# Optimization experiments

Measured on AMD Instinct MI355X. Metric: run time of the kernel, lower is better.

The kernel has to match this reference:

```python
import jax, jax.numpy as jnp
import numpy as np

B, L, C = 128, 1000, 12      # batch, seq_len, input_channels
H = 128                       # lstm_hidden
DM, DS, DC = 128, 16, 4       # d_model, d_state, d_conv
DI = 2 * DM                   # d_inner = expand * d_model
DR = 8                        # dt_rank = ceil(d_model/16)
FC, NC = 128, 5               # fc_hidden_size, num_classes


def setup_inputs() -> dict:
    key = jax.random.key(0)
    ks = jax.random.split(key, 24)
    def rn(k, shape, fan):
        return jax.random.normal(k, shape, jnp.float32) / np.sqrt(fan)
    inp = {}
    inp["x"] = jax.random.normal(ks[0], (B, L, C), jnp.float32)
    # LSTM (single layer, batch_first) — PyTorch gate order i,f,g,o
    inp["W_ih"] = rn(ks[1], (4 * H, C), H)
    inp["W_hh"] = rn(ks[2], (4 * H, H), H)
    inp["b_ih"] = rn(ks[3], (4 * H,), H)
    inp["b_hh"] = rn(ks[4], (4 * H,), H)
    # input_proj: Linear(H, DM)
    inp["Wp"] = rn(ks[5], (DM, H), H)
    inp["bp"] = rn(ks[6], (DM,), H)
    # Mamba params
    inp["in_proj_w"] = rn(ks[7], (2 * DI, DM), DM)
    inp["conv_w"] = rn(ks[8], (DI, 1, DC), DC)        # depthwise conv kernel
    inp["conv_b"] = rn(ks[9], (DI,), DC)
    inp["x_proj_w"] = rn(ks[10], (DR + 2 * DS, DI), DI)
    inp["dt_proj_w"] = rn(ks[11], (DI, DR), DR)
    inp["dt_proj_b"] = rn(ks[12], (DI,), DR)
    inp["A_log"] = jnp.broadcast_to(jnp.log(jnp.arange(1, DS + 1, dtype=jnp.float32)), (DI, DS)).copy()
    inp["D"] = jnp.ones((DI,), jnp.float32)
    inp["out_proj_w"] = rn(ks[13], (DM, DI), DI)
    # classifier head
    inp["fc1_w"] = rn(ks[14], (FC, DM), DM)
    inp["fc1_b"] = rn(ks[15], (FC,), DM)
    inp["fc2_w"] = rn(ks[16], (NC, FC), FC)
    inp["fc2_b"] = rn(ks[17], (NC,), FC)
    return inp


def _lstm(x, W_ih, W_hh, b_ih, b_hh):
    b = b_ih + b_hh
    xg = jnp.einsum('blc,gc->blg', x, W_ih) + b  # precompute input gates (B,L,4H)
    def step(carry, xt):
        h, c = carry
        g = xt + h @ W_hh.T
        i, f, gg, o = jnp.split(g, 4, axis=-1)
        c = jax.nn.sigmoid(f) * c + jax.nn.sigmoid(i) * jnp.tanh(gg)
        h = jax.nn.sigmoid(o) * jnp.tanh(c)
        return (h, c), h
    h0 = jnp.zeros((x.shape[0], H), x.dtype)
    (_, _), hs = jax.lax.scan(step, (h0, h0), jnp.swapaxes(xg, 0, 1))
    return jnp.swapaxes(hs, 0, 1)  # (B,L,H)


def _mamba(u, in_proj_w, conv_w, conv_b, x_proj_w, dt_proj_w, dt_proj_b, A_log, D, out_proj_w):
    xz = jnp.einsum('bld,ed->ble', u, in_proj_w)           # (B,L,2*DI)
    xi, z = jnp.split(xz, 2, axis=-1)
    # causal depthwise conv1d over time
    xc = jnp.swapaxes(xi, 1, 2)                             # (B,DI,L)
    xc = jax.lax.conv_general_dilated(xc, conv_w, (1,), [(DC - 1, 0)],
                                      feature_group_count=DI,
                                      dimension_numbers=('NCH', 'OIH', 'NCH'))
    xc = xc + conv_b[None, :, None]
    xs = jax.nn.silu(jnp.swapaxes(xc, 1, 2))                # (B,L,DI)
    x_dbl = jnp.einsum('bld,ed->ble', xs, x_proj_w)         # (B,L,DR+2*DS)
    dt, Bm, Cm = jnp.split(x_dbl, [DR, DR + DS], axis=-1)
    delta = jax.nn.softplus(jnp.einsum('blr,dr->bld', dt, dt_proj_w) + dt_proj_b)  # (B,L,DI)
    A = -jnp.exp(A_log)                                     # (DI,DS)
    def step(h, inp):
        d_t, B_t, C_t, x_t = inp                            # (B,DI),(B,DS),(B,DS),(B,DI)
        dA = jnp.exp(d_t[:, :, None] * A)                   # (B,DI,DS)
        h = dA * h + (d_t * x_t)[:, :, None] * B_t[:, None, :]
        y = jnp.einsum('bds,bs->bd', h, C_t)
        return h, y
    h0 = jnp.zeros((u.shape[0], DI, DS), u.dtype)
    seq = (jnp.swapaxes(delta, 0, 1), jnp.swapaxes(Bm, 0, 1),
           jnp.swapaxes(Cm, 0, 1), jnp.swapaxes(xs, 0, 1))
    _, ys = jax.lax.scan(step, h0, seq)                     # (L,B,DI)
    y = jnp.swapaxes(ys, 0, 1) + xs * D
    y = y * jax.nn.silu(z)
    return jnp.einsum('bld,ed->ble', y, out_proj_w)         # (B,L,DM)


def reference(x, W_ih, W_hh, b_ih, b_hh, Wp, bp, in_proj_w, conv_w, conv_b,
              x_proj_w, dt_proj_w, dt_proj_b, A_log, D, out_proj_w,
              fc1_w, fc1_b, fc2_w, fc2_b):
    h = _lstm(x, W_ih, W_hh, b_ih, b_hh)
    m_in = jnp.einsum('blh,dh->bld', h, Wp) + bp
    m_out = _mamba(m_in, in_proj_w, conv_w, conv_b, x_proj_w,
                   dt_proj_w, dt_proj_b, A_log, D, out_proj_w)
    pooled = m_out.mean(axis=1)                             # (B,DM)
    hfc = jax.nn.relu(pooled @ fc1_w.T + fc1_b)             # dropout: eval mode (identity)
    return hfc @ fc2_w.T + fc2_b                            # (B,NC)
```

## Files before the change

kernel.cpp:

```cpp
#include <hip/hip_runtime.h>
#include <cstdint>
#include <cstddef>

constexpr int LSEQ = 1000;
constexpr int NB   = 128;
constexpr int CINP = 12;
constexpr int HID  = 128;
constexpr int NGATE = 4 * HID;
constexpr int DMOD = 128;
constexpr int DINN = 256;
constexpr int NCL  = 5;

typedef unsigned short ushort_t;
typedef _Float16 half2_t __attribute__((ext_vector_type(2)));

__device__ __forceinline__ float bf2f(ushort_t u) {
  uint32_t b = ((uint32_t)u) << 16;
  float f; __builtin_memcpy(&f, &b, 4); return f;
}
__device__ __forceinline__ ushort_t f2bf(float f) {
  uint32_t b; __builtin_memcpy(&b, &f, 4);
  uint32_t r = (b + 0x7fffu + ((b >> 16) & 1u)) >> 16;
  return (ushort_t)r;
}
__device__ __forceinline__ half2_t u2h2(uint32_t v) {
  half2_t h; __builtin_memcpy(&h, &v, 4); return h;
}
__device__ __forceinline__ uint32_t h22u(half2_t h) {
  uint32_t v; __builtin_memcpy(&v, &h, 4); return v;
}
__device__ __forceinline__ uint32_t bfpair_to_h2(uint32_t v) {
  half2_t h;
  h.x = (_Float16)bf2f((ushort_t)(v & 0xffff));
  h.y = (_Float16)bf2f((ushort_t)(v >> 16));
  return h22u(h);
}

#if __has_builtin(__builtin_amdgcn_fdot2)
__device__ __forceinline__ float FDOT2(half2_t a, half2_t b, float c) {
  return __builtin_amdgcn_fdot2(a, b, c, false);
}
#else
__device__ __forceinline__ float FDOT2(half2_t a, half2_t b, float c) {
  return c + (float)a.x * (float)b.x + (float)a.y * (float)b.y;
}
#endif

__device__ __forceinline__ void bar_lgkm() {
  asm volatile("s_waitcnt lgkmcnt(0)\n\ts_barrier" ::: "memory");
}

__global__ __launch_bounds__(256) void k0_weff(
    const float* __restrict__ ipw, const float* __restrict__ Wp,
    const float* __restrict__ bp, uint32_t* __restrict__ Weffh,
    float* __restrict__ beff) {
  int idx = blockIdx.x * 256 + threadIdx.x;
  if (idx < NGATE * 64) {
    int e = idx >> 6, j = idx & 63;
    float a0 = 0.f, a1 = 0.f;
    for (int d = 0; d < DMOD; ++d) {
      float w = ipw[e * DMOD + d];
      a0 += w * Wp[d * HID + 2 * j];
      a1 += w * Wp[d * HID + 2 * j + 1];
    }
    half2_t h; h.x = (_Float16)a0; h.y = (_Float16)a1;
    Weffh[idx] = h22u(h);
  }
  if (idx < NGATE) {
    float acc = 0.f;
    for (int d = 0; d < DMOD; ++d) acc += ipw[idx * DMOD + d] * bp[d];
    beff[idx] = acc;
  }
}

__global__ __launch_bounds__(256, 1) void k1_lstm(
    const float* __restrict__ x, const float* __restrict__ W_ih,
    const float* __restrict__ W_hh, const float* __restrict__ b_ih,
    const float* __restrict__ b_hh, ushort_t* __restrict__ hout) {
  __shared__ __align__(16) float x_sh[LSEQ * CINP];
  __shared__ __align__(16) ushort_t h_sh[HID];
  __shared__ float tg_sh[HID];
  __shared__ float so_sh[HID];
  const int t = threadIdx.x;
  const int u = t & 127;
  const int half = t >> 7;
  const int rA = u + half * 256;
  const int rB = rA + 128;
  const int b = blockIdx.x;

  const float4* xg4 = reinterpret_cast<const float4*>(x + (size_t)b * LSEQ * CINP);
  float4* xs4 = reinterpret_cast<float4*>(x_sh);
  for (int i = t; i < LSEQ * CINP / 4; i += 256) xs4[i] = xg4[i];

  half2_t wa2[64], wb2[64];
  {
    const float4* wa4 = reinterpret_cast<const float4*>(W_hh) + rA * (HID / 4);
    const float4* wb4 = reinterpret_cast<const float4*>(W_hh) + rB * (HID / 4);
#pragma unroll
    for (int k = 0; k < HID / 4; ++k) {
      float4 v = wa4[k];
      half2_t a; a.x = (_Float16)v.x; a.y = (_Float16)v.y;
      half2_t c; c.x = (_Float16)v.z; c.y = (_Float16)v.w;
      wa2[2 * k] = a; wa2[2 * k + 1] = c;
      float4 w = wb4[k];
      half2_t d; d.x = (_Float16)w.x; d.y = (_Float16)w.y;
      half2_t e; e.x = (_Float16)w.z; e.y = (_Float16)w.w;
      wb2[2 * k] = d; wb2[2 * k + 1] = e;
    }
  }
  float wia[CINP], wib[CINP];
#pragma unroll
  for (int c = 0; c < CINP; ++c) {
    wia[c] = W_ih[rA * CINP + c];
    wib[c] = W_ih[rB * CINP + c];
  }
  const float biasA = b_ih[rA] + b_hh[rA];
  const float biasB = b_ih[rB] + b_hh[rB];

  float cstate = 0.f;
  if (t < HID) h_sh[t] = 0;
  __syncthreads();

  for (int l = 0; l < LSEQ; ++l) {
    const float* xr = &x_sh[l * CINP];
    float pa0 = biasA, pa1 = 0.f, pa2 = 0.f, pa3 = 0.f;
    float pb0 = biasB, pb1 = 0.f, pb2 = 0.f, pb3 = 0.f;
#pragma unroll
    for (int c = 0; c < CINP; c += 4) {
      float x0 = xr[c], x1 = xr[c + 1], x2 = xr[c + 2], x3 = xr[c + 3];
      pa0 += x0 * wia[c];     pa1 += x1 * wia[c + 1];
      pa2 += x2 * wia[c + 2]; pa3 += x3 * wia[c + 3];
      pb0 += x0 * wib[c];     pb1 += x1 * wib[c + 1];
      pb2 += x2 * wib[c + 2]; pb3 += x3 * wib[c + 3];
    }
    const uint4* h4 = reinterpret_cast<const uint4*>(h_sh);
#pragma unroll
    for (int kk = 0; kk < 16; ++kk) {
      uint4 hv = h4[kk];
      half2_t h0 = u2h2(hv.x), h1 = u2h2(hv.y), h2 = u2h2(hv.z), h3 = u2h2(hv.w);
      pa0 = FDOT2(h0, wa2[4 * kk],     pa0);
      pa1 = FDOT2(h1, wa2[4 * kk + 1], pa1);
      pa2 = FDOT2(h2, wa2[4 * kk + 2], pa2);
      pa3 = FDOT2(h3, wa2[4 * kk + 3], pa3);
      pb0 = FDOT2(h0, wb2[4 * kk],     pb0);
      pb1 = FDOT2(h1, wb2[4 * kk + 1], pb1);
      pb2 = FDOT2(h2, wb2[4 * kk + 2], pb2);
      pb3 = FDOT2(h3, wb2[4 * kk + 3], pb3);
    }
    float gA = (pa0 + pa1) + (pa2 + pa3);
    float gB = (pb0 + pb1) + (pb2 + pb3);

    float si = 0.f, sf = 0.f;
    if (half) {
      float tg = 1.f - 2.f / (__expf(2.f * gA) + 1.f);
      float so = 1.f / (1.f + __expf(-gB));
      tg_sh[u] = tg;
      so_sh[u] = so;
    } else {
      si = 1.f / (1.f + __expf(-gA));
      sf = 1.f / (1.f + __expf(-gB));
    }
    bar_lgkm();
    if (!half) {
      cstate = sf * cstate + si * tg_sh[u];
      float th = 1.f - 2.f / (__expf(2.f * cstate) + 1.f);
      float hv = so_sh[u] * th;
      _Float16 hh = (_Float16)hv;
      ushort_t hb; __builtin_memcpy(&hb, &hh, 2);
      h_sh[u] = hb;
      hout[((size_t)b * LSEQ + l) * HID + u] = f2bf(hv);
    }
    bar_lgkm();
  }
}

__global__ __launch_bounds__(256) void k2_xz(
    const ushort_t* __restrict__ hbuf, const uint32_t* __restrict__ Weffh,
    const float* __restrict__ beff, ushort_t* __restrict__ xi,
    ushort_t* __restrict__ sz) {
  constexpr int S = 66;
  __shared__ __align__(16) uint32_t As[64 * S];
  __shared__ __align__(16) uint32_t Bs[64 * S];
  const int tid = threadIdx.x;
  const size_t m0 = (size_t)blockIdx.x * 64;
  const int n0 = blockIdx.y * 64;

  const uint4* h4g = reinterpret_cast<const uint4*>(hbuf);
  for (int i = tid; i < 64 * 16; i += 256) {
    int row = i >> 4, c = i & 15;
    uint4 v = h4g[(m0 + row) * 16 + c];
    uint32_t* p = &As[row * S + c * 4];
    p[0] = bfpair_to_h2(v.x); p[1] = bfpair_to_h2(v.y);
    p[2] = bfpair_to_h2(v.z); p[3] = bfpair_to_h2(v.w);
  }
  const uint4* w4g = reinterpret_cast<const uint4*>(Weffh);
  for (int i = tid; i < 64 * 16; i += 256) {
    int row = i >> 4, c = i & 15;
    uint4 v = w4g[(size_t)(n0 + row) * 16 + c];
    uint32_t* p = &Bs[row * S + c * 4];
    p[0] = v.x; p[1] = v.y; p[2] = v.z; p[3] = v.w;
  }
  __syncthreads();

  const int tx = tid & 15, ty = tid >> 4;
  float acc[4][4] = {};
  const uint32_t* ap = &As[(ty * 4) * S];
  const uint32_t* bp = &Bs[(tx * 4) * S];
#pragma unroll 4
  for (int kk = 0; kk < 32; ++kk) {
    uint2 a0 = *reinterpret_cast<const uint2*>(&ap[kk * 2]);
    uint2 a1 = *reinterpret_cast<const uint2*>(&ap[S + kk * 2]);
    uint2 a2 = *reinterpret_cast<const uint2*>(&ap[2 * S + kk * 2]);
    uint2 a3 = *reinterpret_cast<const uint2*>(&ap[3 * S + kk * 2]);
    uint2 b0 = *reinterpret_cast<const uint2*>(&bp[kk * 2]);
    uint2 b1 = *reinterpret_cast<const uint2*>(&bp[S + kk * 2]);
    uint2 b2 = *reinterpret_cast<const uint2*>(&bp[2 * S + kk * 2]);
    uint2 b3 = *reinterpret_cast<const uint2*>(&bp[3 * S + kk * 2]);
    acc[0][0] = FDOT2(u2h2(a0.x), u2h2(b0.x), acc[0][0]);
    acc[0][1] = FDOT2(u2h2(a0.x), u2h2(b1.x), acc[0][1]);
    acc[0][2] = FDOT2(u2h2(a0.x), u2h2(b2.x), acc[0][2]);
    acc[0][3] = FDOT2(u2h2(a0.x), u2h2(b3.x), acc[0][3]);
    acc[1][0] = FDOT2(u2h2(a1.x), u2h2(b0.x), acc[1][0]);
    acc[1][1] = FDOT2(u2h2(a1.x), u2h2(b1.x), acc[1][1]);
    acc[1][2] = FDOT2(u2h2(a1.x), u2h2(b2.x), acc[1][2]);
    acc[1][3] = FDOT2(u2h2(a1.x), u2h2(b3.x), acc[1][3]);
    acc[2][0] = FDOT2(u2h2(a2.x), u2h2(b0.x), acc[2][0]);
    acc[2][1] = FDOT2(u2h2(a2.x), u2h2(b1.x), acc[2][1]);
    acc[2][2] = FDOT2(u2h2(a2.x), u2h2(b2.x), acc[2][2]);
    acc[2][3] = FDOT2(u2h2(a2.x), u2h2(b3.x), acc[2][3]);
    acc[3][0] = FDOT2(u2h2(a3.x), u2h2(b0.x), acc[3][0]);
    acc[3][1] = FDOT2(u2h2(a3.x), u2h2(b1.x), acc[3][1]);
    acc[3][2] = FDOT2(u2h2(a3.x), u2h2(b2.x), acc[3][2]);
    acc[3][3] = FDOT2(u2h2(a3.x), u2h2(b3.x), acc[3][3]);
    acc[0][0] = FDOT2(u2h2(a0.y), u2h2(b0.y), acc[0][0]);
    acc[0][1] = FDOT2(u2h2(a0.y), u2h2(b1.y), acc[0][1]);
    acc[0][2] = FDOT2(u2h2(a0.y), u2h2(b2.y), acc[0][2]);
    acc[0][3] = FDOT2(u2h2(a0.y), u2h2(b3.y), acc[0][3]);
    acc[1][0] = FDOT2(u2h2(a1.y), u2h2(b0.y), acc[1][0]);
    acc[1][1] = FDOT2(u2h2(a1.y), u2h2(b1.y), acc[1][1]);
    acc[1][2] = FDOT2(u2h2(a1.y), u2h2(b2.y), acc[1][2]);
    acc[1][3] = FDOT2(u2h2(a1.y), u2h2(b3.y), acc[1][3]);
    acc[2][0] = FDOT2(u2h2(a2.y), u2h2(b0.y), acc[2][0]);
    acc[2][1] = FDOT2(u2h2(a2.y), u2h2(b1.y), acc[2][1]);
    acc[2][2] = FDOT2(u2h2(a2.y), u2h2(b2.y), acc[2][2]);
    acc[2][3] = FDOT2(u2h2(a2.y), u2h2(b3.y), acc[2][3]);
    acc[3][0] = FDOT2(u2h2(a3.y), u2h2(b0.y), acc[3][0]);
    acc[3][1] = FDOT2(u2h2(a3.y), u2h2(b1.y), acc[3][1]);
    acc[3][2] = FDOT2(u2h2(a3.y), u2h2(b2.y), acc[3][2]);
    acc[3][3] = FDOT2(u2h2(a3.y), u2h2(b3.y), acc[3][3]);
  }

  const int col = n0 + tx * 4;
  float4 be = *reinterpret_cast<const float4*>(&beff[col]);
#pragma unroll
  for (int i = 0; i < 4; ++i) {
    size_t row = m0 + ty * 4 + i;
    float v0 = acc[i][0] + be.x, v1 = acc[i][1] + be.y;
    float v2 = acc[i][2] + be.z, v3 = acc[i][3] + be.w;
    ushort4 o;
    if (n0 < 256) {
      o.x = f2bf(v0); o.y = f2bf(v1); o.z = f2bf(v2); o.w = f2bf(v3);
      *reinterpret_cast<ushort4*>(&xi[row * 256 + col]) = o;
    } else {
      o.x = f2bf(v0 / (1.f + __expf(-v0)));
      o.y = f2bf(v1 / (1.f + __expf(-v1)));
      o.z = f2bf(v2 / (1.f + __expf(-v2)));
      o.w = f2bf(v3 / (1.f + __expf(-v3)));
      *reinterpret_cast<ushort4*>(&sz[row * 256 + (col - 256)]) = o;
    }
  }
}

__global__ __launch_bounds__(256) void k3_conv(
    const ushort_t* __restrict__ xi, const float* __restrict__ cw,
    const float* __restrict__ cb, ushort_t* __restrict__ xs) {
  const int d = threadIdx.x;
  const size_t bl0 = (size_t)blockIdx.x * 4;
  const int l0 = (int)(bl0 % LSEQ);
  float w0 = cw[d * 4], w1 = cw[d * 4 + 1], w2 = cw[d * 4 + 2], w3 = cw[d * 4 + 3];
  const float cbv = cb[d];
  const ushort_t* p = &xi[bl0 * 256 + d];
  float xm3 = (l0 >= 3) ? bf2f(p[-768]) : 0.f;
  float xm2 = (l0 >= 2) ? bf2f(p[-512]) : 0.f;
  float xm1 = (l0 >= 1) ? bf2f(p[-256]) : 0.f;
  float x0 = bf2f(p[0]);
  float x1 = bf2f(p[256]);
  float x2 = bf2f(p[512]);
  float x3 = bf2f(p[768]);
  float o0 = cbv + w0 * xm3 + w1 * xm2 + w2 * xm1 + w3 * x0;
  float o1 = cbv + w0 * xm2 + w1 * xm1 + w2 * x0 + w3 * x1;
  float o2 = cbv + w0 * xm1 + w1 * x0 + w2 * x1 + w3 * x2;
  float o3 = cbv + w0 * x0 + w1 * x1 + w2 * x2 + w3 * x3;
  ushort_t* q = &xs[bl0 * 256 + d];
  q[0]   = f2bf(o0 / (1.f + __expf(-o0)));
  q[256] = f2bf(o1 / (1.f + __expf(-o1)));
  q[512] = f2bf(o2 / (1.f + __expf(-o2)));
  q[768] = f2bf(o3 / (1.f + __expf(-o3)));
}

__global__ __launch_bounds__(256) void k4_xdbl(
    const ushort_t* __restrict__ xs, const float* __restrict__ xpw,
    float* __restrict__ dtg, float* __restrict__ bc) {
  constexpr int XSTR = 134;
  __shared__ __align__(16) uint32_t xsh[64 * XSTR];
  __shared__ __align__(16) uint32_t wsh[40 * 128];
  const int tid = threadIdx.x;
  const size_t r0 = (size_t)blockIdx.x * 64;

  for (int i = tid; i < 64 * 128; i += 256) {
    int row = i >> 7, kk = i & 127;
    uint32_t v = *reinterpret_cast<const uint32_t*>(&xs[(r0 + row) * 256 + kk * 2]);
    xsh[row * XSTR + kk] = bfpair_to_h2(v);
  }
  for (int i = tid; i < 40 * 128; i += 256) {
    int c = i >> 7, kk = i & 127;
    half2_t h;
    h.x = (_Float16)xpw[c * 256 + kk * 2];
    h.y = (_Float16)xpw[c * 256 + kk * 2 + 1];
    wsh[i] = h22u(h);
  }
  __syncthreads();

  const int row = tid & 63;
  const int cg = tid >> 6;
  float acc[10] = {};
  for (int kk2 = 0; kk2 < 64; ++kk2) {
    uint2 xv = *reinterpret_cast<const uint2*>(&xsh[row * XSTR + kk2 * 2]);
    half2_t x0 = u2h2(xv.x), x1 = u2h2(xv.y);
#pragma unroll
    for (int i = 0; i < 10; ++i) {
      uint2 wv = *reinterpret_cast<const uint2*>(&wsh[(cg + 4 * i) * 128 + kk2 * 2]);
      acc[i] = FDOT2(x0, u2h2(wv.x), acc[i]);
      acc[i] = FDOT2(x1, u2h2(wv.y), acc[i]);
    }
  }
#pragma unroll
  for (int i = 0; i < 10; ++i) {
    int c = cg + 4 * i;
    if (c < 8) dtg[(r0 + row) * 8 + c] = acc[i];
    else bc[(r0 + row) * 32 + (c - 8)] = acc[i];
  }
}

__global__ __launch_bounds__(256) void k5_scan(
    const float* __restrict__ dtg, const ushort_t* __restrict__ xs,
    const ushort_t* __restrict__ sz, const float* __restrict__ bc,
    const float* __restrict__ A_log, const float* __restrict__ Dv,
    const float* __restrict__ dtw, const float* __restrict__ dtb,
    float* __restrict__ ysum) {
  const int b  = blockIdx.x >> 3;
  const int d  = ((blockIdx.x & 7) << 5) + (threadIdx.x >> 3);
  const int sg = threadIdx.x & 7;

  const float Aa0 = -__expf(A_log[d * 16 + sg * 2]);
  const float Aa1 = -__expf(A_log[d * 16 + sg * 2 + 1]);
  float w8[8];
#pragma unroll
  for (int r = 0; r < 8; ++r) w8[r] = dtw[d * 8 + r];
  const float db = dtb[d];
  const float DD = Dv[d];

  float h0 = 0.f, h1 = 0.f;
  float acc = 0.f, accD = 0.f;
  const size_t base = (size_t)b * LSEQ;

  float4 dta_c = *reinterpret_cast<const float4*>(&dtg[base * 8]);
  float4 dtb_c = *reinterpret_cast<const float4*>(&dtg[base * 8 + 4]);
  float  xv_c  = bf2f(xs[base * 256 + d]);
  float  zv_c  = bf2f(sz[base * 256 + d]);
  float2 bv_c  = *reinterpret_cast<const float2*>(&bc[base * 32 + sg * 2]);
  float2 cv_c  = *reinterpret_cast<const float2*>(&bc[base * 32 + 16 + sg * 2]);

  for (int l = 0; l < LSEQ; ++l) {
    const size_t nrow = base + ((l + 1 < LSEQ) ? (l + 1) : l);
    float4 dta_n = *reinterpret_cast<const float4*>(&dtg[nrow * 8]);
    float4 dtb_n = *reinterpret_cast<const float4*>(&dtg[nrow * 8 + 4]);
    float  xv_n  = bf2f(xs[nrow * 256 + d]);
    float  zv_n  = bf2f(sz[nrow * 256 + d]);
    float2 bv_n  = *reinterpret_cast<const float2*>(&bc[nrow * 32 + sg * 2]);
    float2 cv_n  = *reinterpret_cast<const float2*>(&bc[nrow * 32 + 16 + sg * 2]);

    float a = db + dta_c.x * w8[0] + dta_c.y * w8[1] + dta_c.z * w8[2] + dta_c.w * w8[3]
                 + dtb_c.x * w8[4] + dtb_c.y * w8[5] + dtb_c.z * w8[6] + dtb_c.w * w8[7];
    float dl = (a > 20.f) ? a : __logf(1.f + __expf(a));
    float dx = dl * xv_c;
    h0 = __expf(dl * Aa0) * h0 + dx * bv_c.x;
    h1 = __expf(dl * Aa1) * h1 + dx * bv_c.y;
    acc += (h0 * cv_c.x + h1 * cv_c.y) * zv_c;
    accD += xv_c * zv_c;

    dta_c = dta_n; dtb_c = dtb_n;
    xv_c = xv_n; zv_c = zv_n; bv_c = bv_n; cv_c = cv_n;
  }
  if (sg == 0) acc += DD * accD;
  acc += __shfl_xor(acc, 1);
  acc += __shfl_xor(acc, 2);
  acc += __shfl_xor(acc, 4);
  if (sg == 0) ysum[b * 256 + d] = acc;
}

__global__ __launch_bounds__(128) void k6_head(
    const float* __restrict__ ysum, const float* __restrict__ opw,
    const float* __restrict__ fc1w, const float* __restrict__ fc1b,
    const float* __restrict__ fc2w, const float* __restrict__ fc2b,
    float* __restrict__ out) {
  __shared__ float ys[256], pool[128], fcs[128];
  const int b = blockIdx.x, t = threadIdx.x;
  for (int i = t; i < 256; i += 128) ys[i] = ysum[b * 256 + i];
  __syncthreads();
  float a = 0.f;
  for (int e = 0; e < 256; ++e) a += opw[t * 256 + e] * ys[e];
  pool[t] = a * (1.0f / (float)LSEQ);
  __syncthreads();
  float a1 = fc1b[t];
  for (int d2 = 0; d2 < 128; ++d2) a1 += fc1w[t * 128 + d2] * pool[d2];
  fcs[t] = fmaxf(a1, 0.f);
  __syncthreads();
  if (t < NCL) {
    float o = fc2b[t];
    for (int f = 0; f < 128; ++f) o += fc2w[t * 128 + f] * fcs[f];
    out[b * NCL + t] = o;
  }
}

extern "C" void kernel_launch(void* const* d_in, const int* in_sizes, int n_in,
                              void* d_out, int out_size, void* d_ws, size_t ws_size,
                              hipStream_t stream) {
  const float* x     = (const float*)d_in[0];
  const float* W_ih  = (const float*)d_in[1];
  const float* W_hh  = (const float*)d_in[2];
  const float* b_ih  = (const float*)d_in[3];
  const float* b_hh  = (const float*)d_in[4];
  const float* Wp    = (const float*)d_in[5];
  const float* bp    = (const float*)d_in[6];
  const float* ipw   = (const float*)d_in[7];
  const float* cw    = (const float*)d_in[8];
  const float* cb    = (const float*)d_in[9];
  const float* xpw   = (const float*)d_in[10];
  const float* dtw   = (const float*)d_in[11];
  const float* dtb   = (const float*)d_in[12];
  const float* A_log = (const float*)d_in[13];
  const float* Dv    = (const float*)d_in[14];
  const float* opw   = (const float*)d_in[15];
  const float* fc1w  = (const float*)d_in[16];
  const float* fc1b  = (const float*)d_in[17];
  const float* fc2w  = (const float*)d_in[18];
  const float* fc2b  = (const float*)d_in[19];
  float* out = (float*)d_out;

  const size_t A_WEFF = 131072;
  const size_t A_BEFF = 4096, A_YSUM = 131072;
  const size_t A_HBUF = (size_t)NB * LSEQ * HID * 2;
  const size_t A_XS   = (size_t)NB * LSEQ * DINN * 2;
  const size_t A_SZ   = A_XS;
  const size_t A_DT   = (size_t)NB * LSEQ * 8 * 4;
  const size_t A_BC   = (size_t)NB * LSEQ * 32 * 4;
  const size_t FIXED_WIDE = A_WEFF + A_BEFF + A_YSUM + A_HBUF + A_XS + A_SZ + A_DT + A_BC;

  int nb_w = 0;
  for (int c = 128; c >= 8; c >>= 1) {
    if (FIXED_WIDE + (size_t)c * LSEQ * DINN * 2 <= ws_size) { nb_w = c; break; }
  }

  if (nb_w > 0) {
    char* p = (char*)d_ws;
    uint32_t* Weffh = (uint32_t*)p; p += A_WEFF;
    float*    beff = (float*)p;    p += A_BEFF;
    float*    ysum = (float*)p;    p += A_YSUM;
    ushort_t* hbuf = (ushort_t*)p; p += A_HBUF;
    ushort_t* xsb  = (ushort_t*)p; p += A_XS;
    ushort_t* szb  = (ushort_t*)p; p += A_SZ;
    float*    dtg  = (float*)p;    p += A_DT;
    float*    bcb  = (float*)p;    p += A_BC;
    ushort_t* xib  = (ushort_t*)p;

    hipLaunchKernelGGL(k0_weff, dim3(128), dim3(256), 0, stream, ipw, Wp, bp, Weffh, beff);
    hipLaunchKernelGGL(k1_lstm, dim3(NB), dim3(256), 0, stream, x, W_ih, W_hh, b_ih, b_hh, hbuf);

    for (int b0 = 0; b0 < NB; b0 += nb_w) {
      const int rows = nb_w * LSEQ;
      const size_t ro = (size_t)b0 * LSEQ;
      hipLaunchKernelGGL(k2_xz, dim3(rows / 64, 8), dim3(256), 0, stream,
                         hbuf + ro * HID, Weffh, beff, xib, szb + ro * DINN);
      hipLaunchKernelGGL(k3_conv, dim3(rows / 4), dim3(256), 0, stream,
                         xib, cw, cb, xsb + ro * DINN);
      hipLaunchKernelGGL(k4_xdbl, dim3(rows / 64), dim3(256), 0, stream,
                         xsb + ro * DINN, xpw, dtg + ro * 8, bcb + ro * 32);
    }
    hipLaunchKernelGGL(k5_scan, dim3(NB * 8), dim3(256), 0, stream,
                       dtg, xsb, szb, bcb, A_log, Dv, dtw, dtb, ysum);
    hipLaunchKernelGGL(k6_head, dim3(NB), dim3(128), 0, stream,
                       ysum, opw, fc1w, fc1b, fc2w, fc2b, out);
    return;
  }

  const size_t FIXED = A_WEFF + A_BEFF + A_YSUM + A_HBUF;
  const size_t PERB = (size_t)LSEQ * DINN * 2 * 3 + (size_t)LSEQ * 8 * 4 + (size_t)LSEQ * 32 * 4;
  int nb = 8;
  for (int c = 128; c >= 8; c >>= 1) {
    if (FIXED + (size_t)c * PERB <= ws_size) { nb = c; break; }
  }
  char* p = (char*)d_ws;
  uint32_t* Weffh = (uint32_t*)p; p += A_WEFF;
  float*    beff = (float*)p;    p += A_BEFF;
  float*    ysum = (float*)p;    p += A_YSUM;
  ushort_t* hbuf = (ushort_t*)p; p += A_HBUF;
  ushort_t* xib  = (ushort_t*)p; p += (size_t)nb * LSEQ * DINN * 2;
  ushort_t* szb  = (ushort_t*)p; p += (size_t)nb * LSEQ * DINN * 2;
  ushort_t* xsb  = (ushort_t*)p; p += (size_t)nb * LSEQ * DINN * 2;
  float*    dtg  = (float*)p;    p += (size_t)nb * LSEQ * 8 * 4;
  float*    bcb  = (float*)p;

  hipLaunchKernelGGL(k0_weff, dim3(128), dim3(256), 0, stream, ipw, Wp, bp, Weffh, beff);
  hipLaunchKernelGGL(k1_lstm, dim3(NB), dim3(256), 0, stream, x, W_ih, W_hh, b_ih, b_hh, hbuf);
  for (int b0 = 0; b0 < NB; b0 += nb) {
    const int rows = nb * LSEQ;
    hipLaunchKernelGGL(k2_xz, dim3(rows / 64, 8), dim3(256), 0, stream,
                       hbuf + (size_t)b0 * LSEQ * HID, Weffh, beff, xib, szb);
    hipLaunchKernelGGL(k3_conv, dim3(rows / 4), dim3(256), 0, stream, xib, cw, cb, xsb);
    hipLaunchKernelGGL(k4_xdbl, dim3(rows / 64), dim3(256), 0, stream, xsb, xpw, dtg, bcb);
    hipLaunchKernelGGL(k5_scan, dim3(nb * 8), dim3(256), 0, stream,
                       dtg, xsb, szb, bcb, A_log, Dv, dtw, dtb, ysum + (size_t)b0 * DINN);
  }
  hipLaunchKernelGGL(k6_head, dim3(NB), dim3(128), 0, stream,
                     ysum, opw, fc1w, fc1b, fc2w, fc2b, out);
}
```

Before: 1.507 ms.

## Fuse depthwise causal conv and SiLU into the x/z projection GEMM epilogue

```diff
diff --git a/kernel.cpp b/kernel.cpp
--- a/kernel.cpp
+++ b/kernel.cpp
@@ -174,13 +174,15 @@
   }
 }
 
-__global__ __launch_bounds__(256) void k2_xz(
+__global__ __launch_bounds__(256) void k2f(
     const ushort_t* __restrict__ hbuf, const uint32_t* __restrict__ Weffh,
-    const float* __restrict__ beff, ushort_t* __restrict__ xi,
+    const float* __restrict__ beff, const float* __restrict__ cw,
+    const float* __restrict__ cb, ushort_t* __restrict__ xs,
     ushort_t* __restrict__ sz) {
   constexpr int S = 66;
-  __shared__ __align__(16) uint32_t As[64 * S];
-  __shared__ __align__(16) uint32_t Bs[64 * S];
+  __shared__ __align__(16) uint32_t smem[2 * 64 * S];
+  uint32_t* As = smem;
+  uint32_t* Bs = smem + 64 * S;
   const int tid = threadIdx.x;
   const size_t m0 = (size_t)blockIdx.x * 64;
   const int n0 = blockIdx.y * 64;
@@ -204,98 +206,132 @@
 
   const int tx = tid & 15, ty = tid >> 4;
   float acc[4][4] = {};
-  const uint32_t* ap = &As[(ty * 4) * S];
-  const uint32_t* bp = &Bs[(tx * 4) * S];
+  {
+    const uint32_t* ap = &As[(ty * 4) * S];
+    const uint32_t* bp = &Bs[(tx * 4) * S];
 #pragma unroll 4
-  for (int kk = 0; kk < 32; ++kk) {
-    uint2 a0 = *reinterpret_cast<const uint2*>(&ap[kk * 2]);
-    uint2 a1 = *reinterpret_cast<const uint2*>(&ap[S + kk * 2]);
-    uint2 a2 = *reinterpret_cast<const uint2*>(&ap[2 * S + kk * 2]);
-    uint2 a3 = *reinterpret_cast<const uint2*>(&ap[3 * S + kk * 2]);
-    uint2 b0 = *reinterpret_cast<const uint2*>(&bp[kk * 2]);
-    uint2 b1 = *reinterpret_cast<const uint2*>(&bp[S + kk * 2]);
-    uint2 b2 = *reinterpret_cast<const uint2*>(&bp[2 * S + kk * 2]);
-    uint2 b3 = *reinterpret_cast<const uint2*>(&bp[3 * S + kk * 2]);
-    acc[0][0] = FDOT2(u2h2(a0.x), u2h2(b0.x), acc[0][0]);
-    acc[0][1] = FDOT2(u2h2(a0.x), u2h2(b1.x), acc[0][1]);
-    acc[0][2] = FDOT2(u2h2(a0.x), u2h2(b2.x), acc[0][2]);
-    acc[0][3] = FDOT2(u2h2(a0.x), u2h2(b3.x), acc[0][3]);
-    acc[1][0] = FDOT2(u2h2(a1.x), u2h2(b0.x), acc[1][0]);
-    acc[1][1] = FDOT2(u2h2(a1.x), u2h2(b1.x), acc[1][1]);
-    acc[1][2] = FDOT2(u2h2(a1.x), u2h2(b2.x), acc[1][2]);
-    acc[1][3] = FDOT2(u2h2(a1.x), u2h2(b3.x), acc[1][3]);
-    acc[2][0] = FDOT2(u2h2(a2.x), u2h2(b0.x), acc[2][0]);
-    acc[2][1] = FDOT2(u2h2(a2.x), u2h2(b1.x), acc[2][1]);
-    acc[2][2] = FDOT2(u2h2(a2.x), u2h2(b2.x), acc[2][2]);
-    acc[2][3] = FDOT2(u2h2(a2.x), u2h2(b3.x), acc[2][3]);
-    acc[3][0] = FDOT2(u2h2(a3.x), u2h2(b0.x), acc[3][0]);
-    acc[3][1] = FDOT2(u2h2(a3.x), u2h2(b1.x), acc[3][1]);
-    acc[3][2] = FDOT2(u2h2(a3.x), u2h2(b2.x), acc[3][2]);
-    acc[3][3] = FDOT2(u2h2(a3.x), u2h2(b3.x), acc[3][3]);
-    acc[0][0] = FDOT2(u2h2(a0.y), u2h2(b0.y), acc[0][0]);
-    acc[0][1] = FDOT2(u2h2(a0.y), u2h2(b1.y), acc[0][1]);
-    acc[0][2] = FDOT2(u2h2(a0.y), u2h2(b2.y), acc[0][2]);
-    acc[0][3] = FDOT2(u2h2(a0.y), u2h2(b3.y), acc[0][3]);
-    acc[1][0] = FDOT2(u2h2(a1.y), u2h2(b0.y), acc[1][0]);
-    acc[1][1] = FDOT2(u2h2(a1.y), u2h2(b1.y), acc[1][1]);
-    acc[1][2] = FDOT2(u2h2(a1.y), u2h2(b2.y), acc[1][2]);
-    acc[1][3] = FDOT2(u2h2(a1.y), u2h2(b3.y), acc[1][3]);
-    acc[2][0] = FDOT2(u2h2(a2.y), u2h2(b0.y), acc[2][0]);
-    acc[2][1] = FDOT2(u2h2(a2.y), u2h2(b1.y), acc[2][1]);
-    acc[2][2] = FDOT2(u2h2(a2.y), u2h2(b2.y), acc[2][2]);
-    acc[2][3] = FDOT2(u2h2(a2.y), u2h2(b3.y), acc[2][3]);
-    acc[3][0] = FDOT2(u2h2(a3.y), u2h2(b0.y), acc[3][0]);
-    acc[3][1] = FDOT2(u2h2(a3.y), u2h2(b1.y), acc[3][1]);
-    acc[3][2] = FDOT2(u2h2(a3.y), u2h2(b2.y), acc[3][2]);
-    acc[3][3] = FDOT2(u2h2(a3.y), u2h2(b3.y), acc[3][3]);
+    for (int kk = 0; kk < 32; ++kk) {
+      uint2 a0 = *reinterpret_cast<const uint2*>(&ap[kk * 2]);
+      uint2 a1 = *reinterpret_cast<const uint2*>(&ap[S + kk * 2]);
+      uint2 a2 = *reinterpret_cast<const uint2*>(&ap[2 * S + kk * 2]);
+      uint2 a3 = *reinterpret_cast<const uint2*>(&ap[3 * S + kk * 2]);
+      uint2 b0 = *reinterpret_cast<const uint2*>(&bp[kk * 2]);
+      uint2 b1 = *reinterpret_cast<const uint2*>(&bp[S + kk * 2]);
+      uint2 b2 = *reinterpret_cast<const uint2*>(&bp[2 * S + kk * 2]);
+      uint2 b3 = *reinterpret_cast<const uint2*>(&bp[3 * S + kk * 2]);
+      acc[0][0] = FDOT2(u2h2(a0.x), u2h2(b0.x), acc[0][0]);
+      acc[0][1] = FDOT2(u2h2(a0.x), u2h2(b1.x), acc[0][1]);
+      acc[0][2] = FDOT2(u2h2(a0.x), u2h2(b2.x), acc[0][2]);
+      acc[0][3] = FDOT2(u2h2(a0.x), u2h2(b3.x), acc[0][3]);
+      acc[1][0] = FDOT2(u2h2(a1.x), u2h2(b0.x), acc[1][0]);
+      acc[1][1] = FDOT2(u2h2(a1.x), u2h2(b1.x), acc[1][1]);
+      acc[1][2] = FDOT2(u2h2(a1.x), u2h2(b2.x), acc[1][2]);
+      acc[1][3] = FDOT2(u2h2(a1.x), u2h2(b3.x), acc[1][3]);
+      acc[2][0] = FDOT2(u2h2(a2.x), u2h2(b0.x), acc[2][0]);
+      acc[2][1] = FDOT2(u2h2(a2.x), u2h2(b1.x), acc[2][1]);
+      acc[2][2] = FDOT2(u2h2(a2.x), u2h2(b2.x), acc[2][2]);
+      acc[2][3] = FDOT2(u2h2(a2.x), u2h2(b3.x), acc[2][3]);
+      acc[3][0] = FDOT2(u2h2(a3.x), u2h2(b0.x), acc[3][0]);
+      acc[3][1] = FDOT2(u2h2(a3.x), u2h2(b1.x), acc[3][1]);
+      acc[3][2] = FDOT2(u2h2(a3.x), u2h2(b2.x), acc[3][2]);
+      acc[3][3] = FDOT2(u2h2(a3.x), u2h2(b3.x), acc[3][3]);
+      acc[0][0] = FDOT2(u2h2(a0.y), u2h2(b0.y), acc[0][0]);
+      acc[0][1] = FDOT2(u2h2(a0.y), u2h2(b1.y), acc[0][1]);
+      acc[0][2] = FDOT2(u2h2(a0.y), u2h2(b2.y), acc[0][2]);
+      acc[0][3] = FDOT2(u2h2(a0.y), u2h2(b3.y), acc[0][3]);
+      acc[1][0] = FDOT2(u2h2(a1.y), u2h2(b0.y), acc[1][0]);
+      acc[1][1] = FDOT2(u2h2(a1.y), u2h2(b1.y), acc[1][1]);
+      acc[1][2] = FDOT2(u2h2(a1.y), u2h2(b2.y), acc[1][2]);
+      acc[1][3] = FDOT2(u2h2(a1.y), u2h2(b3.y), acc[1][3]);
+      acc[2][0] = FDOT2(u2h2(a2.y), u2h2(b0.y), acc[2][0]);
+      acc[2][1] = FDOT2(u2h2(a2.y), u2h2(b1.y), acc[2][1]);
+      acc[2][2] = FDOT2(u2h2(a2.y), u2h2(b2.y), acc[2][2]);
+      acc[2][3] = FDOT2(u2h2(a2.y), u2h2(b3.y), acc[2][3]);
+      acc[3][0] = FDOT2(u2h2(a3.y), u2h2(b0.y), acc[3][0]);
+      acc[3][1] = FDOT2(u2h2(a3.y), u2h2(b1.y), acc[3][1]);
+      acc[3][2] = FDOT2(u2h2(a3.y), u2h2(b2.y), acc[3][2]);
+      acc[3][3] = FDOT2(u2h2(a3.y), u2h2(b3.y), acc[3][3]);
+    }
   }
 
   const int col = n0 + tx * 4;
   float4 be = *reinterpret_cast<const float4*>(&beff[col]);
-#pragma unroll
-  for (int i = 0; i < 4; ++i) {
-    size_t row = m0 + ty * 4 + i;
-    float v0 = acc[i][0] + be.x, v1 = acc[i][1] + be.y;
-    float v2 = acc[i][2] + be.z, v3 = acc[i][3] + be.w;
-    ushort4 o;
-    if (n0 < 256) {
-      o.x = f2bf(v0); o.y = f2bf(v1); o.z = f2bf(v2); o.w = f2bf(v3);
-      *reinterpret_cast<ushort4*>(&xi[row * 256 + col]) = o;
-    } else {
+
+  if (n0 >= 256) {
+#pragma unroll
+    for (int i = 0; i < 4; ++i) {
+      size_t row = m0 + ty * 4 + i;
+      float v0 = acc[i][0] + be.x, v1 = acc[i][1] + be.y;
+      float v2 = acc[i][2] + be.z, v3 = acc[i][3] + be.w;
+      ushort4 o;
       o.x = f2bf(v0 / (1.f + __expf(-v0)));
       o.y = f2bf(v1 / (1.f + __expf(-v1)));
       o.z = f2bf(v2 / (1.f + __expf(-v2)));
       o.w = f2bf(v3 / (1.f + __expf(-v3)));
       *reinterpret_cast<ushort4*>(&sz[row * 256 + (col - 256)]) = o;
     }
-  }
-}
-
-__global__ __launch_bounds__(256) void k3_conv(
-    const ushort_t* __restrict__ xi, const float* __restrict__ cw,
-    const float* __restrict__ cb, ushort_t* __restrict__ xs) {
-  const int d = threadIdx.x;
-  const size_t bl0 = (size_t)blockIdx.x * 4;
-  const int l0 = (int)(bl0 % LSEQ);
-  float w0 = cw[d * 4], w1 = cw[d * 4 + 1], w2 = cw[d * 4 + 2], w3 = cw[d * 4 + 3];
-  const float cbv = cb[d];
-  const ushort_t* p = &xi[bl0 * 256 + d];
-  float xm3 = (l0 >= 3) ? bf2f(p[-768]) : 0.f;
-  float xm2 = (l0 >= 2) ? bf2f(p[-512]) : 0.f;
-  float xm1 = (l0 >= 1) ? bf2f(p[-256]) : 0.f;
-  float x0 = bf2f(p[0]);
-  float x1 = bf2f(p[256]);
-  float x2 = bf2f(p[512]);
-  float x3 = bf2f(p[768]);
-  float o0 = cbv + w0 * xm3 + w1 * xm2 + w2 * xm1 + w3 * x0;
-  float o1 = cbv + w0 * xm2 + w1 * xm1 + w2 * x0 + w3 * x1;
-  float o2 = cbv + w0 * xm1 + w1 * x0 + w2 * x1 + w3 * x2;
-  float o3 = cbv + w0 * x0 + w1 * x1 + w2 * x2 + w3 * x3;
-  ushort_t* q = &xs[bl0 * 256 + d];
-  q[0]   = f2bf(o0 / (1.f + __expf(-o0)));
-  q[256] = f2bf(o1 / (1.f + __expf(-o1)));
-  q[512] = f2bf(o2 / (1.f + __expf(-o2)));
-  q[768] = f2bf(o3 / (1.f + __expf(-o3)));
+    return;
+  }
+
+  float haloval = 0.f;
+  const int hc = tid & 63;
+  if (tid < 192) {
+    int hr = tid >> 6;
+    long hrow = (long)m0 - 3 + hr;
+    if (hrow < 0) hrow = 0;
+    const uint4* hg = reinterpret_cast<const uint4*>(hbuf + (size_t)hrow * 128);
+    const uint32_t* brow = &Bs[hc * S];
+    float a0 = beff[n0 + hc], a1 = 0.f, a2 = 0.f, a3 = 0.f;
+#pragma unroll
+    for (int k = 0; k < 16; ++k) {
+      uint4 hv = hg[k];
+      a0 = FDOT2(u2h2(bfpair_to_h2(hv.x)), u2h2(brow[4 * k]),     a0);
+      a1 = FDOT2(u2h2(bfpair_to_h2(hv.y)), u2h2(brow[4 * k + 1]), a1);
+      a2 = FDOT2(u2h2(bfpair_to_h2(hv.z)), u2h2(brow[4 * k + 2]), a2);
+      a3 = FDOT2(u2h2(bfpair_to_h2(hv.w)), u2h2(brow[4 * k + 3]), a3);
+    }
+    haloval = (a0 + a1) + (a2 + a3);
+  }
+  __syncthreads();
+
+  float* X = reinterpret_cast<float*>(smem);
+#pragma unroll
+  for (int i = 0; i < 4; ++i) {
+    int r = ty * 4 + i;
+    float* q = &X[(r + 3) * 68 + tx * 4];
+    q[0] = acc[i][0] + be.x; q[1] = acc[i][1] + be.y;
+    q[2] = acc[i][2] + be.z; q[3] = acc[i][3] + be.w;
+  }
+  if (tid < 192) X[(tid >> 6) * 68 + hc] = haloval;
+  __syncthreads();
+
+  float cw0[4], cw1[4], cw2[4], cw3[4], cbv[4];
+#pragma unroll
+  for (int j = 0; j < 4; ++j) {
+    int d = col + j;
+    cw0[j] = cw[d * 4]; cw1[j] = cw[d * 4 + 1];
+    cw2[j] = cw[d * 4 + 2]; cw3[j] = cw[d * 4 + 3];
+    cbv[j] = cb[d];
+  }
+#pragma unroll
+  for (int i = 0; i < 4; ++i) {
+    int r = ty * 4 + i;
+    size_t m = m0 + r;
+    int l = (int)(m % LSEQ);
+    const float* xr3 = &X[(r + 3) * 68 + tx * 4];
+    ushort_t ov[4];
+#pragma unroll
+    for (int j = 0; j < 4; ++j) {
+      float o0 = cbv[j];
+      o0 += cw3[j] * xr3[j];
+      if (l >= 1) o0 += cw2[j] * xr3[j - 68];
+      if (l >= 2) o0 += cw1[j] * xr3[j - 136];
+      if (l >= 3) o0 += cw0[j] * xr3[j - 204];
+      ov[j] = f2bf(o0 / (1.f + __expf(-o0)));
+    }
+    ushort4 o; o.x = ov[0]; o.y = ov[1]; o.z = ov[2]; o.w = ov[3];
+    *reinterpret_cast<ushort4*>(&xs[m * 256 + col]) = o;
+  }
 }
 
 __global__ __launch_bounds__(256) void k4_xdbl(
@@ -457,12 +493,7 @@
   const size_t A_BC   = (size_t)NB * LSEQ * 32 * 4;
   const size_t FIXED_WIDE = A_WEFF + A_BEFF + A_YSUM + A_HBUF + A_XS + A_SZ + A_DT + A_BC;
 
-  int nb_w = 0;
-  for (int c = 128; c >= 8; c >>= 1) {
-    if (FIXED_WIDE + (size_t)c * LSEQ * DINN * 2 <= ws_size) { nb_w = c; break; }
-  }
-
-  if (nb_w > 0) {
+  if (FIXED_WIDE <= ws_size) {
     char* p = (char*)d_ws;
     uint32_t* Weffh = (uint32_t*)p; p += A_WEFF;
     float*    beff = (float*)p;    p += A_BEFF;
@@ -472,21 +503,14 @@
     ushort_t* szb  = (ushort_t*)p; p += A_SZ;
     float*    dtg  = (float*)p;    p += A_DT;
     float*    bcb  = (float*)p;    p += A_BC;
-    ushort_t* xib  = (ushort_t*)p;
-
+
+    const int rows = NB * LSEQ;
     hipLaunchKernelGGL(k0_weff, dim3(128), dim3(256), 0, stream, ipw, Wp, bp, Weffh, beff);
     hipLaunchKernelGGL(k1_lstm, dim3(NB), dim3(256), 0, stream, x, W_ih, W_hh, b_ih, b_hh, hbuf);
-
-    for (int b0 = 0; b0 < NB; b0 += nb_w) {
-      const int rows = nb_w * LSEQ;
-      const size_t ro = (size_t)b0 * LSEQ;
-      hipLaunchKernelGGL(k2_xz, dim3(rows / 64, 8), dim3(256), 0, stream,
-                         hbuf + ro * HID, Weffh, beff, xib, szb + ro * DINN);
-      hipLaunchKernelGGL(k3_conv, dim3(rows / 4), dim3(256), 0, stream,
-                         xib, cw, cb, xsb + ro * DINN);
-      hipLaunchKernelGGL(k4_xdbl, dim3(rows / 64), dim3(256), 0, stream,
-                         xsb + ro * DINN, xpw, dtg + ro * 8, bcb + ro * 32);
-    }
+    hipLaunchKernelGGL(k2f, dim3(rows / 64, 8), dim3(256), 0, stream,
+                       hbuf, Weffh, beff, cw, cb, xsb, szb);
+    hipLaunchKernelGGL(k4_xdbl, dim3(rows / 64), dim3(256), 0, stream,
+                       xsb, xpw, dtg, bcb);
     hipLaunchKernelGGL(k5_scan, dim3(NB * 8), dim3(256), 0, stream,
                        dtg, xsb, szb, bcb, A_log, Dv, dtw, dtb, ysum);
     hipLaunchKernelGGL(k6_head, dim3(NB), dim3(128), 0, stream,
@@ -495,9 +519,9 @@
   }
 
   const size_t FIXED = A_WEFF + A_BEFF + A_YSUM + A_HBUF;
-  const size_t PERB = (size_t)LSEQ * DINN * 2 * 3 + (size_t)LSEQ * 8 * 4 + (size_t)LSEQ * 32 * 4;
+  const size_t PERB = (size_t)LSEQ * DINN * 2 * 2 + (size_t)LSEQ * 8 * 4 + (size_t)LSEQ * 32 * 4;
   int nb = 8;
-  for (int c = 128; c >= 8; c >>= 1) {
+  for (int c = 64; c >= 8; c >>= 1) {
     if (FIXED + (size_t)c * PERB <= ws_size) { nb = c; break; }
   }
   char* p = (char*)d_ws;
@@ -505,9 +529,8 @@
   float*    beff = (float*)p;    p += A_BEFF;
   float*    ysum = (float*)p;    p += A_YSUM;
   ushort_t* hbuf = (ushort_t*)p; p += A_HBUF;
-  ushort_t* xib  = (ushort_t*)p; p += (size_t)nb * LSEQ * DINN * 2;
+  ushort_t* xsb  = (ushort_t*)p; p += (size_t)nb * LSEQ * DINN * 2;
   ushort_t* szb  = (ushort_t*)p; p += (size_t)nb * LSEQ * DINN * 2;
-  ushort_t* xsb  = (ushort_t*)p; p += (size_t)nb * LSEQ * DINN * 2;
   float*    dtg  = (float*)p;    p += (size_t)nb * LSEQ * 8 * 4;
   float*    bcb  = (float*)p;
 
@@ -515,9 +538,8 @@
   hipLaunchKernelGGL(k1_lstm, dim3(NB), dim3(256), 0, stream, x, W_ih, W_hh, b_ih, b_hh, hbuf);
   for (int b0 = 0; b0 < NB; b0 += nb) {
     const int rows = nb * LSEQ;
-    hipLaunchKernelGGL(k2_xz, dim3(rows / 64, 8), dim3(256), 0, stream,
-                       hbuf + (size_t)b0 * LSEQ * HID, Weffh, beff, xib, szb);
-    hipLaunchKernelGGL(k3_conv, dim3(rows / 4), dim3(256), 0, stream, xib, cw, cb, xsb);
+    hipLaunchKernelGGL(k2f, dim3(rows / 64, 8), dim3(256), 0, stream,
+                       hbuf + (size_t)b0 * LSEQ * HID, Weffh, beff, cw, cb, xsb, szb);
     hipLaunchKernelGGL(k4_xdbl, dim3(rows / 64), dim3(256), 0, stream, xsb, xpw, dtg, bcb);
     hipLaunchKernelGGL(k5_scan, dim3(nb * 8), dim3(256), 0, stream,
                        dtg, xsb, szb, bcb, A_log, Dv, dtw, dtb, ysum + (size_t)b0 * DINN);
```

Result: no change. 1.507 ms (median of 2 runs) (+0.0%).
